# Kernel tuning notes

Measured on AMD Instinct MI355X. Metric: run time of the kernel, lower is better.

The kernel has to match this reference:

```python
import jax, jax.numpy as jnp
import numpy as np

# ---- graph / model config (matches init_kwargs) ----
N_FUNC, N_IN, N_OUT = 10000, 2000, 2000
C = 8          # hidden channels per function node (fix_hidden_channels=True)
K_FF = 16      # function->function in-degree
K_IF = 4       # out-edges per input node
LAYERS = 4     # shared ResBlock applied `layers` times
B = 64
EPS = 1e-5
N_NODES = N_FUNC + N_IN + N_OUT
H = N_FUNC * C


def _build_graph():
    """Homogeneous edge list ordered [f->f, in->f, f->out] like hetero2homo,
    plus COO indices of W1 (E x H) and W3 (H x E) per get_conv_indices."""
    rng = np.random.default_rng(0)
    ff_dst = np.repeat(np.arange(N_FUNC), K_FF)
    ff_src = rng.integers(0, N_FUNC, ff_dst.shape[0])
    if_src = np.repeat(np.arange(N_IN) + N_FUNC, K_IF)
    if_dst = rng.integers(0, N_FUNC, if_src.shape[0])
    fo_dst = np.arange(N_OUT) + N_FUNC + N_IN
    fo_src = rng.integers(0, N_FUNC, N_OUT)
    src = np.concatenate([ff_src, if_src, fo_src]).astype(np.int32)
    dst = np.concatenate([ff_dst, if_dst, fo_dst]).astype(np.int32)
    # W1: edge e (dst = function node j) -> hidden channels j*C + c
    e1 = np.nonzero(dst < N_FUNC)[0]
    w1_row = np.repeat(e1, C).astype(np.int32)
    w1_col = (np.repeat(dst[e1].astype(np.int64), C) * C + np.tile(np.arange(C), e1.shape[0])).astype(np.int32)
    # W3: hidden channel src*C + c -> edge e (src = function node)
    e3 = np.nonzero(src < N_FUNC)[0]
    w3_col = np.repeat(e3, C).astype(np.int32)
    w3_row = (np.repeat(src[e3].astype(np.int64), C) * C + np.tile(np.arange(C), e3.shape[0])).astype(np.int32)
    return src, dst, w1_row, w1_col, w3_row, w3_col


def setup_inputs() -> dict:
    src, dst, w1_row, w1_col, w3_row, w3_col = _build_graph()
    key = jax.random.key(0)
    k0, k1, k2 = jax.random.split(key, 3)
    s1 = 1.0 / np.sqrt(K_FF * C)   # fan-based scale for W1 values
    s3 = 1.0 / np.sqrt(C)          # fan-based scale for W3 values
    E = src.shape[0]
    return {
        "x": jax.random.normal(k0, (B, N_IN), jnp.float32),
        "w1_val": jax.random.normal(k1, (w1_row.shape[0],), jnp.float32) * s1,
        "b1": jnp.zeros((H,), jnp.float32),
        "w3_val": jax.random.normal(k2, (w3_row.shape[0],), jnp.float32) * s3,
        "b3": jnp.zeros((E,), jnp.float32),
        "gamma": jnp.ones((H,), jnp.float32),
        "beta": jnp.zeros((H,), jnp.float32),
        "edge_src": jnp.asarray(src),
        "edge_dst": jnp.asarray(dst),
        "w1_row": jnp.asarray(w1_row),
        "w1_col": jnp.asarray(w1_col),
        "w3_row": jnp.asarray(w3_row),
        "w3_col": jnp.asarray(w3_col),
    }


def _sparse_linear(xin, row, col, val, bias, out_dim):
    # out[b, j] = sum_{(i,j) in nz} W[i,j] * x[b,i] + bias[j]
    contrib = xin[:, row] * val                      # [B, nnz]
    out = jnp.zeros((xin.shape[0], out_dim), xin.dtype).at[:, col].add(contrib)
    return out + bias


def _group_layernorm(h, gamma, beta):
    # fix_hidden_channels=True => equal-size groups of C channels per function node
    g = h.reshape(h.shape[0], N_FUNC, C)
    mu = g.mean(-1, keepdims=True)
    var = g.var(-1, keepdims=True)
    g = (g - mu) * jax.lax.rsqrt(var + EPS)
    return g.reshape(h.shape[0], -1) * gamma + beta


def reference(x, w1_val, b1, w3_val, b3, gamma, beta,
              edge_src, edge_dst, w1_row, w1_col, w3_row, w3_col):
    E = edge_src.shape[0]
    # node values -> edge values (node2edge gathers source-node value per edge)
    x_node = jnp.zeros((x.shape[0], N_NODES), x.dtype).at[:, N_FUNC:N_FUNC + N_IN].set(x)
    xe = x_node[:, edge_src]                          # [B, E]

    def block(xe):  # ResBlock: lin1 -> GroupLayerNorm -> GELU -> lin3 -> +residual
        h = _sparse_linear(xe, w1_row, w1_col, w1_val, b1, H)
        h = _group_layernorm(h, gamma, beta)
        h = jax.nn.gelu(h, approximate=False)
        return _sparse_linear(h, w3_row, w3_col, w3_val, b3, E) + xe

    for _ in range(LAYERS):  # share_layers=True: same weights each layer
        xe = block(xe)
    xe = xe / LAYERS

    # edge2node: each output node has exactly one incoming edge (the last N_OUT edges)
    out_idx = edge_dst[-N_OUT:] - (N_FUNC + N_IN)
    out = jnp.zeros((xe.shape[0], N_OUT), xe.dtype).at[:, out_idx].set(xe[:, -N_OUT:])
    return out
```

## Files before the change

### kernel.cpp

```cpp
#include <hip/hip_runtime.h>

#define N_FUNC 10000
#define N_IN   2000
#define N_OUT  2000
#define CCH    8
#define K_FF   16
#define E_TOTAL 170000
#define E_FF    160000
#define E_W1    168000
#define E_IF    8000
#define BATCH   64
#define N_LAYERS 4
#define EPS_LN  1e-5f
#define IF_CAP  16
#define HROW    (BATCH * CCH)

typedef float f2 __attribute__((ext_vector_type(2)));

__device__ __forceinline__ f2 bfpair(unsigned int u) {
    f2 r;
    r.x = __builtin_bit_cast(float, u << 16);
    r.y = __builtin_bit_cast(float, u & 0xffff0000u);
    return r;
}
__device__ __forceinline__ unsigned int bfpack2(float f0, float f1) {
    unsigned int x0 = __builtin_bit_cast(unsigned int, f0);
    unsigned int x1 = __builtin_bit_cast(unsigned int, f1);
    unsigned int r0 = (x0 + 0x7fffu + ((x0 >> 16) & 1u)) >> 16;
    unsigned int r1 = (x1 + 0x7fffu + ((x1 >> 16) & 1u)) & 0xffff0000u;
    return r0 | r1;
}

__device__ __forceinline__ float fast_gelu(float x) {
    float x2 = x * x;
    float u  = x * __builtin_fmaf(0.044715f, x2, 1.0f);
    float e  = exp2f(-2.3022080f * u);
    return x * (1.0f / (1.0f + e));
}


__global__ void fill_prep(const int* __restrict__ dst, const float* __restrict__ x,
                          int* __restrict__ if_cnt, int* __restrict__ if_bkt,
                          float* __restrict__ xT) {
    int i = blockIdx.x * blockDim.x + threadIdx.x;
    if (i < E_IF) {
        int e = E_FF + i;
        int d = dst[e];
        int pos = atomicAdd(&if_cnt[d], 1);
        if_bkt[d * IF_CAP + pos] = e;
    }
    if (i < N_IN * BATCH) {
        int col = i >> 6, lane = i & 63;
        xT[col * BATCH + lane] = x[lane * N_IN + col];
    }
}


__device__ __forceinline__ void if_accum(
        f2* __restrict__ acc2, const float* __restrict__ xT,
        const float* __restrict__ w1, const float* __restrict__ b3,
        const int* __restrict__ if_cnt, const int* __restrict__ if_bkt,
        int f, int lane, float lf) {
    int icnt = if_cnt[f];
    for (int j = 0; j < icnt; j++) {
        int e = if_bkt[f * IF_CAP + j];
        int ii = (e - E_FF) >> 2;
        float xv = xT[ii * BATCH + lane] + lf * b3[e];
        f2 xv2; xv2.x = xv; xv2.y = xv;
        const f2* w1v = (const f2*)(w1 + (size_t)e * CCH);
        #pragma unroll
        for (int q = 0; q < 4; q++) acc2[q] += xv2 * w1v[q];
    }
}

__device__ __forceinline__ void ln_gelu(
        const f2* __restrict__ acc2, const float* __restrict__ gamma,
        const float* __restrict__ beta, int f, f2* __restrict__ h2) {
    float mu = 0.f;
    #pragma unroll
    for (int q = 0; q < 4; q++) mu += acc2[q].x + acc2[q].y;
    mu *= 0.125f;
    float var = 0.f;
    #pragma unroll
    for (int q = 0; q < 4; q++) {
        float dx = acc2[q].x - mu, dy = acc2[q].y - mu;
        var += dx * dx + dy * dy;
    }
    var *= 0.125f;
    float rs = rsqrtf(var + EPS_LN);
    const f2* gv = (const f2*)(gamma + (size_t)f * CCH);
    const f2* bv = (const f2*)(beta + (size_t)f * CCH);
    f2 mu2; mu2.x = mu; mu2.y = mu;
    f2 rs2; rs2.x = rs; rs2.y = rs;
    #pragma unroll
    for (int q = 0; q < 4; q++) {
        f2 g = (acc2[q] - mu2) * rs2 * gv[q] + bv[q];
        h2[q].x = fast_gelu(g.x);
        h2[q].y = fast_gelu(g.y);
    }
}

__device__ __forceinline__ void compute_h_gather(
        const unsigned short* __restrict__ Hold, const float* __restrict__ xT,
        const float* __restrict__ w1, const float* __restrict__ b1,
        const float* __restrict__ gamma, const float* __restrict__ beta,
        const float* __restrict__ w3, const float* __restrict__ b3,
        const int* __restrict__ esrc, const int* __restrict__ if_cnt,
        const int* __restrict__ if_bkt, int f, int lane, float lf,
        f2* __restrict__ h2) {
    int srcs[K_FF];
    #pragma unroll
    for (int k = 0; k < K_FF; k++) srcs[k] = esrc[f * K_FF + k];
    uint4 hrow[K_FF];
    #pragma unroll
    for (int k = 0; k < K_FF; k++)
        hrow[k] = *(const uint4*)(Hold + (size_t)srcs[k] * HROW + lane * CCH);

    const f2* b1v = (const f2*)(b1 + (size_t)f * CCH);
    f2 acc2[4];
    #pragma unroll
    for (int q = 0; q < 4; q++) acc2[q] = b1v[q];

    #pragma unroll
    for (int k = 0; k < K_FF; k++) {
        int e = f * K_FF + k;
        const f2* w3v = (const f2*)(w3 + (size_t)e * CCH);
        const f2* w1v = (const f2*)(w1 + (size_t)e * CCH);
        f2 d = bfpair(hrow[k].x) * w3v[0];
        d += bfpair(hrow[k].y) * w3v[1];
        d += bfpair(hrow[k].z) * w3v[2];
        d += bfpair(hrow[k].w) * w3v[3];
        float xv = d.x + d.y + lf * b3[e];
        f2 xv2; xv2.x = xv; xv2.y = xv;
        #pragma unroll
        for (int q = 0; q < 4; q++) acc2[q] += xv2 * w1v[q];
    }
    if_accum(acc2, xT, w1, b3, if_cnt, if_bkt, f, lane, lf);
    ln_gelu(acc2, gamma, beta, f, h2);
}


__global__ __launch_bounds__(256, 4) void block_first(
        unsigned short* __restrict__ Hnew, const float* __restrict__ xT,
        const float* __restrict__ w1, const float* __restrict__ b1,
        const float* __restrict__ gamma, const float* __restrict__ beta,
        const float* __restrict__ b3, const int* __restrict__ if_cnt,
        const int* __restrict__ if_bkt) {
    int wid = (blockIdx.x * blockDim.x + threadIdx.x) >> 6;
    int lane = threadIdx.x & 63;
    int f = __builtin_amdgcn_readfirstlane(wid);
    if (f >= N_FUNC) return;
    const f2* b1v = (const f2*)(b1 + (size_t)f * CCH);
    f2 acc2[4];
    #pragma unroll
    for (int q = 0; q < 4; q++) acc2[q] = b1v[q];
    if_accum(acc2, xT, w1, b3, if_cnt, if_bkt, f, lane, 0.0f);
    f2 h2[4];
    ln_gelu(acc2, gamma, beta, f, h2);
    uint4 o;
    o.x = bfpack2(h2[0].x, h2[0].y); o.y = bfpack2(h2[1].x, h2[1].y);
    o.z = bfpack2(h2[2].x, h2[2].y); o.w = bfpack2(h2[3].x, h2[3].y);
    *(uint4*)(Hnew + (size_t)f * HROW + lane * CCH) = o;
}


__global__ __launch_bounds__(256, 4) void block_mid(
        const unsigned short* __restrict__ Hold, unsigned short* __restrict__ Hnew,
        const float* __restrict__ xT, const float* __restrict__ w1,
        const float* __restrict__ b1, const float* __restrict__ gamma,
        const float* __restrict__ beta, const float* __restrict__ w3,
        const float* __restrict__ b3, const int* __restrict__ esrc,
        const int* __restrict__ if_cnt, const int* __restrict__ if_bkt, float lf) {
    int wid = (blockIdx.x * blockDim.x + threadIdx.x) >> 6;
    int lane = threadIdx.x & 63;
    int f = __builtin_amdgcn_readfirstlane(wid);
    if (f >= N_FUNC) return;
    uint4 own = *(const uint4*)(Hold + (size_t)f * HROW + lane * CCH);
    f2 h2[4];
    compute_h_gather(Hold, xT, w1, b1, gamma, beta, w3, b3, esrc,
                     if_cnt, if_bkt, f, lane, lf, h2);
    f2 s0 = bfpair(own.x) + h2[0];
    f2 s1 = bfpair(own.y) + h2[1];
    f2 s2 = bfpair(own.z) + h2[2];
    f2 s3 = bfpair(own.w) + h2[3];
    uint4 o;
    o.x = bfpack2(s0.x, s0.y); o.y = bfpack2(s1.x, s1.y);
    o.z = bfpack2(s2.x, s2.y); o.w = bfpack2(s3.x, s3.y);
    *(uint4*)(Hnew + (size_t)f * HROW + lane * CCH) = o;
}


__global__ __launch_bounds__(256, 4) void block_out(
        const unsigned short* __restrict__ Hold, const float* __restrict__ xT,
        const float* __restrict__ w1, const float* __restrict__ b1,
        const float* __restrict__ gamma, const float* __restrict__ beta,
        const float* __restrict__ w3, const float* __restrict__ b3,
        const int* __restrict__ esrc, const int* __restrict__ if_cnt,
        const int* __restrict__ if_bkt, float* __restrict__ out) {
    int wid = (blockIdx.x * blockDim.x + threadIdx.x) >> 6;
    int lane = threadIdx.x & 63;
    int j = __builtin_amdgcn_readfirstlane(wid);
    if (j >= N_OUT) return;
    int e = E_W1 + j;
    int s = __builtin_amdgcn_readfirstlane(esrc[e]);

    uint4 own = *(const uint4*)(Hold + (size_t)s * HROW + lane * CCH);
    f2 h2[4];
    compute_h_gather(Hold, xT, w1, b1, gamma, beta, w3, b3, esrc,
                     if_cnt, if_bkt, s, lane, 3.0f, h2);
    f2 Hf0 = bfpair(own.x) + h2[0];
    f2 Hf1 = bfpair(own.y) + h2[1];
    f2 Hf2 = bfpair(own.z) + h2[2];
    f2 Hf3 = bfpair(own.w) + h2[3];

    int p = e - E_IF;
    const f2* w3v = (const f2*)(w3 + (size_t)p * CCH);
    f2 a = Hf0 * w3v[0];
    a += Hf1 * w3v[1];
    a += Hf2 * w3v[2];
    a += Hf3 * w3v[3];
    out[lane * N_OUT + j] = b3[e] + 0.25f * (a.x + a.y);
}


extern "C" void kernel_launch(void* const* d_in, const int* in_sizes, int n_in,
                              void* d_out, int out_size, void* d_ws, size_t ws_size,
                              hipStream_t stream) {
    const float* x      = (const float*)d_in[0];
    const float* w1_val = (const float*)d_in[1];
    const float* b1     = (const float*)d_in[2];
    const float* w3_val = (const float*)d_in[3];
    const float* b3     = (const float*)d_in[4];
    const float* gamma  = (const float*)d_in[5];
    const float* beta   = (const float*)d_in[6];
    const int* edge_src = (const int*)d_in[7];
    const int* edge_dst = (const int*)d_in[8];
    float* out = (float*)d_out;

    char* base = (char*)d_ws;
    size_t off = 0;
    auto alloc = [&](size_t bytes) -> void* {
        void* p = base + off;
        off += (bytes + 255) & ~(size_t)255;
        return p;
    };
    unsigned short* HsumA = (unsigned short*)alloc((size_t)N_FUNC * HROW * 2);
    unsigned short* HsumB = (unsigned short*)alloc((size_t)N_FUNC * HROW * 2);
    float* xT    = (float*)alloc((size_t)N_IN * BATCH * 4);
    int* if_cnt  = (int*)alloc(N_FUNC * 4);
    int* if_bkt  = (int*)alloc((size_t)N_FUNC * IF_CAP * 4);
    (void)ws_size; (void)in_sizes; (void)n_in; (void)out_size;

    hipMemsetAsync(if_cnt, 0, N_FUNC * 4, stream);
    fill_prep<<<(N_IN * BATCH + 255) / 256, 256, 0, stream>>>(
        edge_dst, x, if_cnt, if_bkt, xT);

    block_first<<<(N_FUNC * BATCH) / 256, 256, 0, stream>>>(
        HsumA, xT, w1_val, b1, gamma, beta, b3, if_cnt, if_bkt);
    block_mid<<<(N_FUNC * BATCH) / 256, 256, 0, stream>>>(
        HsumA, HsumB, xT, w1_val, b1, gamma, beta, w3_val, b3,
        edge_src, if_cnt, if_bkt, 1.0f);
    block_mid<<<(N_FUNC * BATCH) / 256, 256, 0, stream>>>(
        HsumB, HsumA, xT, w1_val, b1, gamma, beta, w3_val, b3,
        edge_src, if_cnt, if_bkt, 2.0f);
    block_out<<<(N_OUT * BATCH) / 256, 256, 0, stream>>>(
        HsumA, xT, w1_val, b1, gamma, beta, w3_val, b3,
        edge_src, if_cnt, if_bkt, out);
}
```

Baseline: 171.8 us.

## Split gather into source-side edge value kernel with pruning for output layer

Adds a CSR-style out-edge bucket per source node and a new edge_vals kernel. Each source reads its bf16 hidden row once, computes the W3 edge values for all its outgoing edges, and writes them to an fp32 buffer. The mid and output blocks then read these contiguous per-edge values instead of gathering 16 random hidden rows per destination. In the last layer only edges feeding the needed output sources are computed. The trade is extra kernel launches, a 41MB fp32 round trip through memory per layer, and atomic bucket construction.

```diff
diff --git a/kernel.cpp b/kernel.cpp
--- a/kernel.cpp
+++ b/kernel.cpp
@@ -13,6 +13,7 @@
 #define N_LAYERS 4
 #define EPS_LN  1e-5f
 #define IF_CAP  16
+#define OUT_CAP 64
 #define HROW    (BATCH * CCH)
 
 typedef float f2 __attribute__((ext_vector_type(2)));
@@ -39,10 +40,17 @@
 }
 
 
-__global__ void fill_prep(const int* __restrict__ dst, const float* __restrict__ x,
+__global__ void fill_prep(const int* __restrict__ src, const int* __restrict__ dst,
+                          const float* __restrict__ x,
                           int* __restrict__ if_cnt, int* __restrict__ if_bkt,
-                          float* __restrict__ xT) {
+                          int* __restrict__ out_cnt, int* __restrict__ out_bkt,
+                          int* __restrict__ needed, float* __restrict__ xT) {
     int i = blockIdx.x * blockDim.x + threadIdx.x;
+    if (i < E_FF) {
+        int s = src[i];
+        int pos = atomicAdd(&out_cnt[s], 1);
+        out_bkt[s * OUT_CAP + pos] = i;
+    }
     if (i < E_IF) {
         int e = E_FF + i;
         int d = dst[e];
@@ -52,6 +60,9 @@
     if (i < N_IN * BATCH) {
         int col = i >> 6, lane = i & 63;
         xT[col * BATCH + lane] = x[lane * N_IN + col];
+    }
+    if (i < N_OUT) {
+        needed[src[E_W1 + i]] = 1;
     }
 }
 
@@ -100,21 +111,17 @@
     }
 }
 
-__device__ __forceinline__ void compute_h_gather(
-        const unsigned short* __restrict__ Hold, const float* __restrict__ xT,
+__device__ __forceinline__ void compute_h_from_v(
+        const float* __restrict__ v, const float* __restrict__ xT,
         const float* __restrict__ w1, const float* __restrict__ b1,
         const float* __restrict__ gamma, const float* __restrict__ beta,
-        const float* __restrict__ w3, const float* __restrict__ b3,
-        const int* __restrict__ esrc, const int* __restrict__ if_cnt,
+        const float* __restrict__ b3, const int* __restrict__ if_cnt,
         const int* __restrict__ if_bkt, int f, int lane, float lf,
         f2* __restrict__ h2) {
-    int srcs[K_FF];
-    #pragma unroll
-    for (int k = 0; k < K_FF; k++) srcs[k] = esrc[f * K_FF + k];
-    uint4 hrow[K_FF];
+    float xv[K_FF];
     #pragma unroll
     for (int k = 0; k < K_FF; k++)
-        hrow[k] = *(const uint4*)(Hold + (size_t)srcs[k] * HROW + lane * CCH);
+        xv[k] = v[(size_t)(f * K_FF + k) * BATCH + lane];
 
     const f2* b1v = (const f2*)(b1 + (size_t)f * CCH);
     f2 acc2[4];
@@ -123,20 +130,43 @@
 
     #pragma unroll
     for (int k = 0; k < K_FF; k++) {
-        int e = f * K_FF + k;
-        const f2* w3v = (const f2*)(w3 + (size_t)e * CCH);
-        const f2* w1v = (const f2*)(w1 + (size_t)e * CCH);
-        f2 d = bfpair(hrow[k].x) * w3v[0];
-        d += bfpair(hrow[k].y) * w3v[1];
-        d += bfpair(hrow[k].z) * w3v[2];
-        d += bfpair(hrow[k].w) * w3v[3];
-        float xv = d.x + d.y + lf * b3[e];
-        f2 xv2; xv2.x = xv; xv2.y = xv;
+        const f2* w1v = (const f2*)(w1 + (size_t)(f * K_FF + k) * CCH);
+        f2 xv2; xv2.x = xv[k]; xv2.y = xv[k];
         #pragma unroll
         for (int q = 0; q < 4; q++) acc2[q] += xv2 * w1v[q];
     }
     if_accum(acc2, xT, w1, b3, if_cnt, if_bkt, f, lane, lf);
     ln_gelu(acc2, gamma, beta, f, h2);
+}
+
+
+__global__ __launch_bounds__(256, 4) void edge_vals(
+        const unsigned short* __restrict__ Hold, const float* __restrict__ w3,
+        const float* __restrict__ b3, const int* __restrict__ out_cnt,
+        const int* __restrict__ out_bkt, const int* __restrict__ needed,
+        float* __restrict__ v, float lf, int prune) {
+    int wid = (blockIdx.x * blockDim.x + threadIdx.x) >> 6;
+    int lane = threadIdx.x & 63;
+    int s = __builtin_amdgcn_readfirstlane(wid);
+    if (s >= N_FUNC) return;
+    int cnt = out_cnt[s];
+    if (cnt == 0) return;
+    uint4 hr = *(const uint4*)(Hold + (size_t)s * HROW + lane * CCH);
+    f2 h0 = bfpair(hr.x), h1 = bfpair(hr.y), h2 = bfpair(hr.z), h3 = bfpair(hr.w);
+    int base = s * OUT_CAP;
+    int e = __builtin_amdgcn_readfirstlane(out_bkt[base]);
+    for (int j = 0; j < cnt; j++) {
+        int e_nxt = __builtin_amdgcn_readfirstlane(out_bkt[base + j + 1]);
+        if (!prune || needed[e >> 4]) {
+            const f2* w3v = (const f2*)(w3 + (size_t)e * CCH);
+            f2 d = h0 * w3v[0];
+            d += h1 * w3v[1];
+            d += h2 * w3v[2];
+            d += h3 * w3v[3];
+            v[(size_t)e * BATCH + lane] = __builtin_fmaf(lf, b3[e], d.x + d.y);
+        }
+        e = e_nxt;
+    }
 }
 
 
@@ -164,21 +194,21 @@
 }
 
 
-__global__ __launch_bounds__(256, 4) void block_mid(
+__global__ __launch_bounds__(256, 4) void block_mid_v(
         const unsigned short* __restrict__ Hold, unsigned short* __restrict__ Hnew,
-        const float* __restrict__ xT, const float* __restrict__ w1,
-        const float* __restrict__ b1, const float* __restrict__ gamma,
-        const float* __restrict__ beta, const float* __restrict__ w3,
-        const float* __restrict__ b3, const int* __restrict__ esrc,
-        const int* __restrict__ if_cnt, const int* __restrict__ if_bkt, float lf) {
+        const float* __restrict__ v, const float* __restrict__ xT,
+        const float* __restrict__ w1, const float* __restrict__ b1,
+        const float* __restrict__ gamma, const float* __restrict__ beta,
+        const float* __restrict__ b3, const int* __restrict__ if_cnt,
+        const int* __restrict__ if_bkt, float lf) {
     int wid = (blockIdx.x * blockDim.x + threadIdx.x) >> 6;
     int lane = threadIdx.x & 63;
     int f = __builtin_amdgcn_readfirstlane(wid);
     if (f >= N_FUNC) return;
     uint4 own = *(const uint4*)(Hold + (size_t)f * HROW + lane * CCH);
     f2 h2[4];
-    compute_h_gather(Hold, xT, w1, b1, gamma, beta, w3, b3, esrc,
-                     if_cnt, if_bkt, f, lane, lf, h2);
+    compute_h_from_v(v, xT, w1, b1, gamma, beta, b3, if_cnt, if_bkt,
+                     f, lane, lf, h2);
     f2 s0 = bfpair(own.x) + h2[0];
     f2 s1 = bfpair(own.y) + h2[1];
     f2 s2 = bfpair(own.z) + h2[2];
@@ -190,13 +220,14 @@
 }
 
 
-__global__ __launch_bounds__(256, 4) void block_out(
-        const unsigned short* __restrict__ Hold, const float* __restrict__ xT,
-        const float* __restrict__ w1, const float* __restrict__ b1,
-        const float* __restrict__ gamma, const float* __restrict__ beta,
-        const float* __restrict__ w3, const float* __restrict__ b3,
-        const int* __restrict__ esrc, const int* __restrict__ if_cnt,
-        const int* __restrict__ if_bkt, float* __restrict__ out) {
+__global__ __launch_bounds__(256, 4) void block_out_v(
+        const unsigned short* __restrict__ Hold, const float* __restrict__ v,
+        const float* __restrict__ xT, const float* __restrict__ w1,
+        const float* __restrict__ b1, const float* __restrict__ gamma,
+        const float* __restrict__ beta, const float* __restrict__ w3,
+        const float* __restrict__ b3, const int* __restrict__ esrc,
+        const int* __restrict__ if_cnt, const int* __restrict__ if_bkt,
+        float* __restrict__ out) {
     int wid = (blockIdx.x * blockDim.x + threadIdx.x) >> 6;
     int lane = threadIdx.x & 63;
     int j = __builtin_amdgcn_readfirstlane(wid);
@@ -206,8 +237,8 @@
 
     uint4 own = *(const uint4*)(Hold + (size_t)s * HROW + lane * CCH);
     f2 h2[4];
-    compute_h_gather(Hold, xT, w1, b1, gamma, beta, w3, b3, esrc,
-                     if_cnt, if_bkt, s, lane, 3.0f, h2);
+    compute_h_from_v(v, xT, w1, b1, gamma, beta, b3, if_cnt, if_bkt,
+                     s, lane, 3.0f, h2);
     f2 Hf0 = bfpair(own.x) + h2[0];
     f2 Hf1 = bfpair(own.y) + h2[1];
     f2 Hf2 = bfpair(own.z) + h2[2];
@@ -247,23 +278,35 @@
     unsigned short* HsumA = (unsigned short*)alloc((size_t)N_FUNC * HROW * 2);
     unsigned short* HsumB = (unsigned short*)alloc((size_t)N_FUNC * HROW * 2);
     float* xT    = (float*)alloc((size_t)N_IN * BATCH * 4);
-    int* if_cnt  = (int*)alloc(N_FUNC * 4);
+    int*   cnts  = (int*)alloc((size_t)3 * N_FUNC * 4);
+    int* if_cnt  = cnts;
+    int* out_cnt = cnts + N_FUNC;
+    int* needed  = cnts + 2 * N_FUNC;
     int* if_bkt  = (int*)alloc((size_t)N_FUNC * IF_CAP * 4);
+    int* out_bkt = (int*)alloc((size_t)N_FUNC * OUT_CAP * 4);
+    float* v     = (float*)alloc((size_t)E_FF * BATCH * 4);
     (void)ws_size; (void)in_sizes; (void)n_in; (void)out_size;
 
-    hipMemsetAsync(if_cnt, 0, N_FUNC * 4, stream);
-    fill_prep<<<(N_IN * BATCH + 255) / 256, 256, 0, stream>>>(
-        edge_dst, x, if_cnt, if_bkt, xT);
+    hipMemsetAsync(cnts, 0, (size_t)3 * N_FUNC * 4, stream);
+    fill_prep<<<(E_FF + 255) / 256, 256, 0, stream>>>(
+        edge_src, edge_dst, x, if_cnt, if_bkt, out_cnt, out_bkt, needed, xT);
 
     block_first<<<(N_FUNC * BATCH) / 256, 256, 0, stream>>>(
         HsumA, xT, w1_val, b1, gamma, beta, b3, if_cnt, if_bkt);
-    block_mid<<<(N_FUNC * BATCH) / 256, 256, 0, stream>>>(
-        HsumA, HsumB, xT, w1_val, b1, gamma, beta, w3_val, b3,
-        edge_src, if_cnt, if_bkt, 1.0f);
-    block_mid<<<(N_FUNC * BATCH) / 256, 256, 0, stream>>>(
-        HsumB, HsumA, xT, w1_val, b1, gamma, beta, w3_val, b3,
-        edge_src, if_cnt, if_bkt, 2.0f);
-    block_out<<<(N_OUT * BATCH) / 256, 256, 0, stream>>>(
-        HsumA, xT, w1_val, b1, gamma, beta, w3_val, b3,
+
+    edge_vals<<<(N_FUNC * BATCH) / 256, 256, 0, stream>>>(
+        HsumA, w3_val, b3, out_cnt, out_bkt, needed, v, 1.0f, 0);
+    block_mid_v<<<(N_FUNC * BATCH) / 256, 256, 0, stream>>>(
+        HsumA, HsumB, v, xT, w1_val, b1, gamma, beta, b3, if_cnt, if_bkt, 1.0f);
+
+    edge_vals<<<(N_FUNC * BATCH) / 256, 256, 0, stream>>>(
+        HsumB, w3_val, b3, out_cnt, out_bkt, needed, v, 2.0f, 0);
+    block_mid_v<<<(N_FUNC * BATCH) / 256, 256, 0, stream>>>(
+        HsumB, HsumA, v, xT, w1_val, b1, gamma, beta, b3, if_cnt, if_bkt, 2.0f);
+
+    edge_vals<<<(N_FUNC * BATCH) / 256, 256, 0, stream>>>(
+        HsumA, w3_val, b3, out_cnt, out_bkt, needed, v, 3.0f, 1);
+    block_out_v<<<(N_OUT * BATCH) / 256, 256, 0, stream>>>(
+        HsumA, v, xT, w1_val, b1, gamma, beta, w3_val, b3,
         edge_src, if_cnt, if_bkt, out);
 }
```

Measured after the change: 231.8 us. +34.9%, slower.

## Shard function-node work across eight waves, one batch-channel element per lane

Applied to the files above, without the earlier changes.

The mid and output kernels now split each function node's 64x8 hidden row across 8 wavefronts (shards). Each lane handles a single (batch, channel) element and uses cross-lane shuffles within groups of 8 for the W3 dot product and the layer-norm statistics. Before, one wave did the whole row and each lane held 8 channels. The aim is more parallelism and higher occupancy (launch bounds raised to 8) with fewer registers per lane. In exchange, edge indices and weights are loaded redundantly by 8x more waves, the gathers are narrower 2-byte loads, and shuffle overhead is added.

```diff
diff --git a/kernel.cpp b/kernel.cpp
--- a/kernel.cpp
+++ b/kernel.cpp
@@ -5,15 +5,14 @@
 #define N_OUT  2000
 #define CCH    8
 #define K_FF   16
-#define E_TOTAL 170000
 #define E_FF    160000
 #define E_W1    168000
 #define E_IF    8000
 #define BATCH   64
-#define N_LAYERS 4
 #define EPS_LN  1e-5f
 #define IF_CAP  16
 #define HROW    (BATCH * CCH)
+#define NSHARD  8
 
 typedef float f2 __attribute__((ext_vector_type(2)));
 
@@ -30,12 +29,26 @@
     unsigned int r1 = (x1 + 0x7fffu + ((x1 >> 16) & 1u)) & 0xffff0000u;
     return r0 | r1;
 }
+__device__ __forceinline__ unsigned short bf1(float f) {
+    unsigned int x = __builtin_bit_cast(unsigned int, f);
+    return (unsigned short)((x + 0x7fffu + ((x >> 16) & 1u)) >> 16);
+}
+__device__ __forceinline__ float unbf1(unsigned short u) {
+    return __builtin_bit_cast(float, (unsigned int)u << 16);
+}
 
 __device__ __forceinline__ float fast_gelu(float x) {
     float x2 = x * x;
     float u  = x * __builtin_fmaf(0.044715f, x2, 1.0f);
     float e  = exp2f(-2.3022080f * u);
     return x * (1.0f / (1.0f + e));
+}
+
+__device__ __forceinline__ float reduce8(float t) {
+    t += __shfl_xor(t, 1);
+    t += __shfl_xor(t, 2);
+    t += __shfl_xor(t, 4);
+    return t;
 }
 
 
@@ -100,43 +113,49 @@
     }
 }
 
-__device__ __forceinline__ void compute_h_gather(
+
+__device__ __forceinline__ float compute_h_shard(
         const unsigned short* __restrict__ Hold, const float* __restrict__ xT,
         const float* __restrict__ w1, const float* __restrict__ b1,
         const float* __restrict__ gamma, const float* __restrict__ beta,
         const float* __restrict__ w3, const float* __restrict__ b3,
         const int* __restrict__ esrc, const int* __restrict__ if_cnt,
-        const int* __restrict__ if_bkt, int f, int lane, float lf,
-        f2* __restrict__ h2) {
+        const int* __restrict__ if_bkt, int f, int shard, int lane, float lf) {
+    int c  = lane & 7;
+    int bg = shard * 8 + (lane >> 3);
+    int e0 = f * K_FF;
+
     int srcs[K_FF];
     #pragma unroll
-    for (int k = 0; k < K_FF; k++) srcs[k] = esrc[f * K_FF + k];
-    uint4 hrow[K_FF];
+    for (int k = 0; k < K_FF; k++) srcs[k] = esrc[e0 + k];
+
+    float hk[K_FF];
     #pragma unroll
     for (int k = 0; k < K_FF; k++)
-        hrow[k] = *(const uint4*)(Hold + (size_t)srcs[k] * HROW + lane * CCH);
-
-    const f2* b1v = (const f2*)(b1 + (size_t)f * CCH);
-    f2 acc2[4];
-    #pragma unroll
-    for (int q = 0; q < 4; q++) acc2[q] = b1v[q];
-
+        hk[k] = unbf1(Hold[(size_t)srcs[k] * HROW + shard * 64 + lane]);
+
+    float acc = b1[(size_t)f * CCH + c];
     #pragma unroll
     for (int k = 0; k < K_FF; k++) {
-        int e = f * K_FF + k;
-        const f2* w3v = (const f2*)(w3 + (size_t)e * CCH);
-        const f2* w1v = (const f2*)(w1 + (size_t)e * CCH);
-        f2 d = bfpair(hrow[k].x) * w3v[0];
-        d += bfpair(hrow[k].y) * w3v[1];
-        d += bfpair(hrow[k].z) * w3v[2];
-        d += bfpair(hrow[k].w) * w3v[3];
-        float xv = d.x + d.y + lf * b3[e];
-        f2 xv2; xv2.x = xv; xv2.y = xv;
-        #pragma unroll
-        for (int q = 0; q < 4; q++) acc2[q] += xv2 * w1v[q];
-    }
-    if_accum(acc2, xT, w1, b3, if_cnt, if_bkt, f, lane, lf);
-    ln_gelu(acc2, gamma, beta, f, h2);
+        int e = e0 + k;
+        float t  = hk[k] * w3[(size_t)e * CCH + c];
+        float xv = reduce8(t) + lf * b3[e];
+        acc = __builtin_fmaf(xv, w1[(size_t)e * CCH + c], acc);
+    }
+    int icnt = if_cnt[f];
+    for (int j = 0; j < icnt; j++) {
+        int e = if_bkt[f * IF_CAP + j];
+        int ii = (e - E_FF) >> 2;
+        float xv = xT[ii * BATCH + bg] + lf * b3[e];
+        acc = __builtin_fmaf(xv, w1[(size_t)e * CCH + c], acc);
+    }
+    float mu = reduce8(acc) * 0.125f;
+    float d  = acc - mu;
+    float var = reduce8(d * d) * 0.125f;
+    float rs = rsqrtf(var + EPS_LN);
+    float g = __builtin_fmaf(d * rs, gamma[(size_t)f * CCH + c],
+                             beta[(size_t)f * CCH + c]);
+    return fast_gelu(g);
 }
 
 
@@ -164,62 +183,46 @@
 }
 
 
-__global__ __launch_bounds__(256, 4) void block_mid(
+__global__ __launch_bounds__(256, 8) void block_mid_s(
         const unsigned short* __restrict__ Hold, unsigned short* __restrict__ Hnew,
         const float* __restrict__ xT, const float* __restrict__ w1,
         const float* __restrict__ b1, const float* __restrict__ gamma,
         const float* __restrict__ beta, const float* __restrict__ w3,
         const float* __restrict__ b3, const int* __restrict__ esrc,
         const int* __restrict__ if_cnt, const int* __restrict__ if_bkt, float lf) {
-    int wid = (blockIdx.x * blockDim.x + threadIdx.x) >> 6;
-    int lane = threadIdx.x & 63;
-    int f = __builtin_amdgcn_readfirstlane(wid);
-    if (f >= N_FUNC) return;
-    uint4 own = *(const uint4*)(Hold + (size_t)f * HROW + lane * CCH);
-    f2 h2[4];
-    compute_h_gather(Hold, xT, w1, b1, gamma, beta, w3, b3, esrc,
-                     if_cnt, if_bkt, f, lane, lf, h2);
-    f2 s0 = bfpair(own.x) + h2[0];
-    f2 s1 = bfpair(own.y) + h2[1];
-    f2 s2 = bfpair(own.z) + h2[2];
-    f2 s3 = bfpair(own.w) + h2[3];
-    uint4 o;
-    o.x = bfpack2(s0.x, s0.y); o.y = bfpack2(s1.x, s1.y);
-    o.z = bfpack2(s2.x, s2.y); o.w = bfpack2(s3.x, s3.y);
-    *(uint4*)(Hnew + (size_t)f * HROW + lane * CCH) = o;
-}
-
-
-__global__ __launch_bounds__(256, 4) void block_out(
+    int shard = blockIdx.x & 7;
+    int lane  = threadIdx.x & 63;
+    int f = __builtin_amdgcn_readfirstlane((blockIdx.x >> 3) * 4 + (threadIdx.x >> 6));
+    size_t oidx = (size_t)f * HROW + shard * 64 + lane;
+    float own = unbf1(Hold[oidx]);
+    float h = compute_h_shard(Hold, xT, w1, b1, gamma, beta, w3, b3,
+                              esrc, if_cnt, if_bkt, f, shard, lane, lf);
+    Hnew[oidx] = bf1(own + h);
+}
+
+
+__global__ __launch_bounds__(256, 8) void block_out_s(
         const unsigned short* __restrict__ Hold, const float* __restrict__ xT,
         const float* __restrict__ w1, const float* __restrict__ b1,
         const float* __restrict__ gamma, const float* __restrict__ beta,
         const float* __restrict__ w3, const float* __restrict__ b3,
         const int* __restrict__ esrc, const int* __restrict__ if_cnt,
         const int* __restrict__ if_bkt, float* __restrict__ out) {
-    int wid = (blockIdx.x * blockDim.x + threadIdx.x) >> 6;
-    int lane = threadIdx.x & 63;
-    int j = __builtin_amdgcn_readfirstlane(wid);
-    if (j >= N_OUT) return;
+    int shard = blockIdx.x & 7;
+    int lane  = threadIdx.x & 63;
+    int j = __builtin_amdgcn_readfirstlane((blockIdx.x >> 3) * 4 + (threadIdx.x >> 6));
     int e = E_W1 + j;
     int s = __builtin_amdgcn_readfirstlane(esrc[e]);
 
-    uint4 own = *(const uint4*)(Hold + (size_t)s * HROW + lane * CCH);
-    f2 h2[4];
-    compute_h_gather(Hold, xT, w1, b1, gamma, beta, w3, b3, esrc,
-                     if_cnt, if_bkt, s, lane, 3.0f, h2);
-    f2 Hf0 = bfpair(own.x) + h2[0];
-    f2 Hf1 = bfpair(own.y) + h2[1];
-    f2 Hf2 = bfpair(own.z) + h2[2];
-    f2 Hf3 = bfpair(own.w) + h2[3];
+    float own = unbf1(Hold[(size_t)s * HROW + shard * 64 + lane]);
+    float h = compute_h_shard(Hold, xT, w1, b1, gamma, beta, w3, b3,
+                              esrc, if_cnt, if_bkt, s, shard, lane, 3.0f);
+    float Hf = own + h;
 
     int p = e - E_IF;
-    const f2* w3v = (const f2*)(w3 + (size_t)p * CCH);
-    f2 a = Hf0 * w3v[0];
-    a += Hf1 * w3v[1];
-    a += Hf2 * w3v[2];
-    a += Hf3 * w3v[3];
-    out[lane * N_OUT + j] = b3[e] + 0.25f * (a.x + a.y);
+    float a = reduce8(Hf * w3[(size_t)p * CCH + (lane & 7)]);
+    if ((lane & 7) == 0)
+        out[(size_t)(shard * 8 + (lane >> 3)) * N_OUT + j] = b3[e] + 0.25f * a;
 }
 
 
@@ -252,18 +255,22 @@
     (void)ws_size; (void)in_sizes; (void)n_in; (void)out_size;
 
     hipMemsetAsync(if_cnt, 0, N_FUNC * 4, stream);
+
     fill_prep<<<(N_IN * BATCH + 255) / 256, 256, 0, stream>>>(
         edge_dst, x, if_cnt, if_bkt, xT);
 
     block_first<<<(N_FUNC * BATCH) / 256, 256, 0, stream>>>(
         HsumA, xT, w1_val, b1, gamma, beta, b3, if_cnt, if_bkt);
-    block_mid<<<(N_FUNC * BATCH) / 256, 256, 0, stream>>>(
+
+    block_mid_s<<<NSHARD * (N_FUNC / 4), 256, 0, stream>>>(
         HsumA, HsumB, xT, w1_val, b1, gamma, beta, w3_val, b3,
         edge_src, if_cnt, if_bkt, 1.0f);
-    block_mid<<<(N_FUNC * BATCH) / 256, 256, 0, stream>>>(
+
+    block_mid_s<<<NSHARD * (N_FUNC / 4), 256, 0, stream>>>(
         HsumB, HsumA, xT, w1_val, b1, gamma, beta, w3_val, b3,
         edge_src, if_cnt, if_bkt, 2.0f);
-    block_out<<<(N_OUT * BATCH) / 256, 256, 0, stream>>>(
+
+    block_out_s<<<NSHARD * (N_OUT / 4), 256, 0, stream>>>(
         HsumA, xT, w1_val, b1, gamma, beta, w3_val, b3,
         edge_src, if_cnt, if_bkt, out);
 }
```

After: 398.0 us. 2.32x slower.

## Split hidden state into batch-quarter slabs mapped to XCD pairs for L2 locality

Applied to the files above, without the earlier changes.

Reorganizes the bf16 hidden-state buffer into four slabs, each holding 16 batch columns for all function nodes. The middle and output kernels map blocks so that each quarter slab is processed by one pair of XCDs, and each wave covers four function nodes by sixteen batch entries. The goal is to shrink the gather working set per XCD so that random neighbour-row gathers hit in the local L2 instead of going to HBM/MALL. The cost is that each lane now reads per-node weights and indices that were previously wave-uniform, which lowers scalarization, and the launch geometry depends on the hardware block-to-XCD round-robin assignment.

```diff
diff --git a/kernel.cpp b/kernel.cpp
--- a/kernel.cpp
+++ b/kernel.cpp
@@ -5,15 +5,15 @@
 #define N_OUT  2000
 #define CCH    8
 #define K_FF   16
-#define E_TOTAL 170000
 #define E_FF    160000
 #define E_W1    168000
 #define E_IF    8000
 #define BATCH   64
-#define N_LAYERS 4
 #define EPS_LN  1e-5f
 #define IF_CAP  16
 #define HROW    (BATCH * CCH)
+#define QBATCH  16
+#define SLAB    (N_FUNC * QBATCH * CCH)
 
 typedef float f2 __attribute__((ext_vector_type(2)));
 
@@ -60,12 +60,12 @@
         f2* __restrict__ acc2, const float* __restrict__ xT,
         const float* __restrict__ w1, const float* __restrict__ b3,
         const int* __restrict__ if_cnt, const int* __restrict__ if_bkt,
-        int f, int lane, float lf) {
+        int f, int bidx, float lf) {
     int icnt = if_cnt[f];
     for (int j = 0; j < icnt; j++) {
         int e = if_bkt[f * IF_CAP + j];
         int ii = (e - E_FF) >> 2;
-        float xv = xT[ii * BATCH + lane] + lf * b3[e];
+        float xv = xT[ii * BATCH + bidx] + lf * b3[e];
         f2 xv2; xv2.x = xv; xv2.y = xv;
         const f2* w1v = (const f2*)(w1 + (size_t)e * CCH);
         #pragma unroll
@@ -100,21 +100,22 @@
     }
 }
 
-__device__ __forceinline__ void compute_h_gather(
-        const unsigned short* __restrict__ Hold, const float* __restrict__ xT,
+__device__ __forceinline__ void compute_h_gather_q(
+        const unsigned short* __restrict__ Hq, const float* __restrict__ xT,
         const float* __restrict__ w1, const float* __restrict__ b1,
         const float* __restrict__ gamma, const float* __restrict__ beta,
         const float* __restrict__ w3, const float* __restrict__ b3,
         const int* __restrict__ esrc, const int* __restrict__ if_cnt,
-        const int* __restrict__ if_bkt, int f, int lane, float lf,
+        const int* __restrict__ if_bkt, int f, int bq, int bidx, float lf,
         f2* __restrict__ h2) {
+    int e0 = f * K_FF;
     int srcs[K_FF];
     #pragma unroll
-    for (int k = 0; k < K_FF; k++) srcs[k] = esrc[f * K_FF + k];
+    for (int k = 0; k < K_FF; k++) srcs[k] = esrc[e0 + k];
     uint4 hrow[K_FF];
     #pragma unroll
     for (int k = 0; k < K_FF; k++)
-        hrow[k] = *(const uint4*)(Hold + (size_t)srcs[k] * HROW + lane * CCH);
+        hrow[k] = *(const uint4*)(Hq + (size_t)srcs[k] * (QBATCH * CCH) + bq * CCH);
 
     const f2* b1v = (const f2*)(b1 + (size_t)f * CCH);
     f2 acc2[4];
@@ -123,7 +124,7 @@
 
     #pragma unroll
     for (int k = 0; k < K_FF; k++) {
-        int e = f * K_FF + k;
+        int e = e0 + k;
         const f2* w3v = (const f2*)(w3 + (size_t)e * CCH);
         const f2* w1v = (const f2*)(w1 + (size_t)e * CCH);
         f2 d = bfpair(hrow[k].x) * w3v[0];
@@ -135,7 +136,7 @@
         #pragma unroll
         for (int q = 0; q < 4; q++) acc2[q] += xv2 * w1v[q];
     }
-    if_accum(acc2, xT, w1, b3, if_cnt, if_bkt, f, lane, lf);
+    if_accum(acc2, xT, w1, b3, if_cnt, if_bkt, f, bidx, lf);
     ln_gelu(acc2, gamma, beta, f, h2);
 }
 
@@ -160,25 +161,33 @@
     uint4 o;
     o.x = bfpack2(h2[0].x, h2[0].y); o.y = bfpack2(h2[1].x, h2[1].y);
     o.z = bfpack2(h2[2].x, h2[2].y); o.w = bfpack2(h2[3].x, h2[3].y);
-    *(uint4*)(Hnew + (size_t)f * HROW + lane * CCH) = o;
-}
-
-
-__global__ __launch_bounds__(256, 4) void block_mid(
+    int q = lane >> 4, bq = lane & 15;
+    *(uint4*)(Hnew + (size_t)q * SLAB + (size_t)f * (QBATCH * CCH) + bq * CCH) = o;
+}
+
+
+__global__ __launch_bounds__(256, 4) void block_mid_q(
         const unsigned short* __restrict__ Hold, unsigned short* __restrict__ Hnew,
         const float* __restrict__ xT, const float* __restrict__ w1,
         const float* __restrict__ b1, const float* __restrict__ gamma,
         const float* __restrict__ beta, const float* __restrict__ w3,
         const float* __restrict__ b3, const int* __restrict__ esrc,
         const int* __restrict__ if_cnt, const int* __restrict__ if_bkt, float lf) {
-    int wid = (blockIdx.x * blockDim.x + threadIdx.x) >> 6;
+    int blk  = blockIdx.x;
+    int xcd  = blk & 7;
+    int q    = xcd >> 1;
+    int l    = ((blk >> 3) << 1) | (xcd & 1);
     int lane = threadIdx.x & 63;
-    int f = __builtin_amdgcn_readfirstlane(wid);
+    int f    = l * 16 + ((threadIdx.x >> 6) << 2) + (lane >> 4);
+    int bq   = lane & 15;
+    int bidx = q * QBATCH + bq;
     if (f >= N_FUNC) return;
-    uint4 own = *(const uint4*)(Hold + (size_t)f * HROW + lane * CCH);
+    const unsigned short* Hq = Hold + (size_t)q * SLAB;
+    size_t oidx = (size_t)q * SLAB + (size_t)f * (QBATCH * CCH) + bq * CCH;
+    uint4 own = *(const uint4*)(Hold + oidx);
     f2 h2[4];
-    compute_h_gather(Hold, xT, w1, b1, gamma, beta, w3, b3, esrc,
-                     if_cnt, if_bkt, f, lane, lf, h2);
+    compute_h_gather_q(Hq, xT, w1, b1, gamma, beta, w3, b3, esrc,
+                       if_cnt, if_bkt, f, bq, bidx, lf, h2);
     f2 s0 = bfpair(own.x) + h2[0];
     f2 s1 = bfpair(own.y) + h2[1];
     f2 s2 = bfpair(own.z) + h2[2];
@@ -186,40 +195,44 @@
     uint4 o;
     o.x = bfpack2(s0.x, s0.y); o.y = bfpack2(s1.x, s1.y);
     o.z = bfpack2(s2.x, s2.y); o.w = bfpack2(s3.x, s3.y);
-    *(uint4*)(Hnew + (size_t)f * HROW + lane * CCH) = o;
-}
-
-
-__global__ __launch_bounds__(256, 4) void block_out(
+    *(uint4*)(Hnew + oidx) = o;
+}
+
+
+__global__ __launch_bounds__(256, 4) void block_out_q(
         const unsigned short* __restrict__ Hold, const float* __restrict__ xT,
         const float* __restrict__ w1, const float* __restrict__ b1,
         const float* __restrict__ gamma, const float* __restrict__ beta,
         const float* __restrict__ w3, const float* __restrict__ b3,
         const int* __restrict__ esrc, const int* __restrict__ if_cnt,
         const int* __restrict__ if_bkt, float* __restrict__ out) {
-    int wid = (blockIdx.x * blockDim.x + threadIdx.x) >> 6;
+    int blk  = blockIdx.x;
+    int xcd  = blk & 7;
+    int q    = xcd >> 1;
+    int l    = ((blk >> 3) << 1) | (xcd & 1);
     int lane = threadIdx.x & 63;
-    int j = __builtin_amdgcn_readfirstlane(wid);
+    int j    = l * 16 + ((threadIdx.x >> 6) << 2) + (lane >> 4);
+    int bq   = lane & 15;
+    int bidx = q * QBATCH + bq;
     if (j >= N_OUT) return;
     int e = E_W1 + j;
-    int s = __builtin_amdgcn_readfirstlane(esrc[e]);
-
-    uint4 own = *(const uint4*)(Hold + (size_t)s * HROW + lane * CCH);
+    int s = esrc[e];
+    const unsigned short* Hq = Hold + (size_t)q * SLAB;
+    uint4 own = *(const uint4*)(Hq + (size_t)s * (QBATCH * CCH) + bq * CCH);
     f2 h2[4];
-    compute_h_gather(Hold, xT, w1, b1, gamma, beta, w3, b3, esrc,
-                     if_cnt, if_bkt, s, lane, 3.0f, h2);
+    compute_h_gather_q(Hq, xT, w1, b1, gamma, beta, w3, b3, esrc,
+                       if_cnt, if_bkt, s, bq, bidx, 3.0f, h2);
     f2 Hf0 = bfpair(own.x) + h2[0];
     f2 Hf1 = bfpair(own.y) + h2[1];
     f2 Hf2 = bfpair(own.z) + h2[2];
     f2 Hf3 = bfpair(own.w) + h2[3];
-
     int p = e - E_IF;
     const f2* w3v = (const f2*)(w3 + (size_t)p * CCH);
     f2 a = Hf0 * w3v[0];
     a += Hf1 * w3v[1];
     a += Hf2 * w3v[2];
     a += Hf3 * w3v[3];
-    out[lane * N_OUT + j] = b3[e] + 0.25f * (a.x + a.y);
+    out[(size_t)bidx * N_OUT + j] = b3[e] + 0.25f * (a.x + a.y);
 }
 
 
@@ -252,18 +265,22 @@
     (void)ws_size; (void)in_sizes; (void)n_in; (void)out_size;
 
     hipMemsetAsync(if_cnt, 0, N_FUNC * 4, stream);
+
     fill_prep<<<(N_IN * BATCH + 255) / 256, 256, 0, stream>>>(
         edge_dst, x, if_cnt, if_bkt, xT);
 
     block_first<<<(N_FUNC * BATCH) / 256, 256, 0, stream>>>(
         HsumA, xT, w1_val, b1, gamma, beta, b3, if_cnt, if_bkt);
-    block_mid<<<(N_FUNC * BATCH) / 256, 256, 0, stream>>>(
+
+    block_mid_q<<<2504, 256, 0, stream>>>(
         HsumA, HsumB, xT, w1_val, b1, gamma, beta, w3_val, b3,
         edge_src, if_cnt, if_bkt, 1.0f);
-    block_mid<<<(N_FUNC * BATCH) / 256, 256, 0, stream>>>(
+
+    block_mid_q<<<2504, 256, 0, stream>>>(
         HsumB, HsumA, xT, w1_val, b1, gamma, beta, w3_val, b3,
         edge_src, if_cnt, if_bkt, 2.0f);
-    block_out<<<(N_OUT * BATCH) / 256, 256, 0, stream>>>(
+
+    block_out_q<<<512, 256, 0, stream>>>(
         HsumA, xT, w1_val, b1, gamma, beta, w3_val, b3,
         edge_src, if_cnt, if_bkt, out);
 }
```

Result: slower. 192.7 us (+12.2%).
